# Kernel optimization log

Hardware: AMD Instinct MI355X
Metric: run time of the kernel (lower is better)

The kernel has to match this reference:

```python
import jax, jax.numpy as jnp
import numpy as np
from jax import lax

T, N, C, S = 1024, 64, 512, 64
BLANK = 0
STRUCT_TAGS = jnp.array([1, 2, 3, 4, 5, 6, 7, 8], dtype=jnp.int32)
STRUCT_WEIGHT = 1.0
NEG = -1e30


def setup_inputs() -> dict:
    key = jax.random.key(0)
    k1, k2, k3 = jax.random.split(key, 3)
    logits = jax.random.normal(k1, (T, N, C), dtype=jnp.float32)
    log_probs = jax.nn.log_softmax(logits, axis=-1)
    targets = jax.random.randint(k2, (N, S), 1, C, dtype=jnp.int32)  # exclude blank
    input_lengths = jnp.full((N,), T, dtype=jnp.int32)
    target_lengths = jax.random.randint(k3, (N,), 32, S + 1, dtype=jnp.int32)
    return {"log_probs": log_probs, "targets": targets,
            "input_lengths": input_lengths, "target_lengths": target_lengths}


def _is_struct(x):
    return (x[..., None] == STRUCT_TAGS).any(-1)


def _compact(tokens, mask, L):
    # Pack masked tokens to the left, pad with -1. tokens/mask: (N, L) -> (N, L)
    n = tokens.shape[0]
    pos = jnp.cumsum(mask, axis=-1) - 1            # destination slot per kept token
    idx = jnp.where(mask, pos, L)                  # dump masked-out entries in slot L
    out = jnp.full((n, L + 1), -1, dtype=tokens.dtype)
    out = out.at[jnp.arange(n)[:, None], idx].set(jnp.where(mask, tokens, -1))
    return out[:, :L]


def _ctc_loss(log_probs, targets, input_lengths, target_lengths):
    # Extended target: blanks interleaved -> (N, U), U = 2S+1
    U = 2 * S + 1
    ext = jnp.full((N, U), BLANK, dtype=targets.dtype).at[:, 1::2].set(targets)
    # lp[t, n, u] = log_probs[t, n, ext[n, u]]
    lp = log_probs[:, jnp.arange(N)[:, None], ext]                 # (T, N, U)
    ext2 = jnp.concatenate([jnp.full((N, 2), -1, ext.dtype), ext[:, :-2]], 1)
    allow_skip = (ext != BLANK) & (ext != ext2)                    # (N, U)

    a0 = jnp.full((N, U), NEG, dtype=log_probs.dtype)
    a0 = a0.at[:, 0].set(lp[0, :, 0]).at[:, 1].set(lp[0, :, 1])

    def step(a, lp_t):
        a1 = jnp.concatenate([jnp.full((N, 1), NEG, a.dtype), a[:, :-1]], 1)
        a2 = jnp.concatenate([jnp.full((N, 2), NEG, a.dtype), a[:, :-2]], 1)
        a2 = jnp.where(allow_skip, a2, NEG)
        a_new = jnp.logaddexp(jnp.logaddexp(a, a1), a2) + lp_t
        return a_new, a_new

    _, alphas = lax.scan(step, a0, lp[1:])
    alphas = jnp.concatenate([a0[None], alphas], 0)                # (T, N, U)

    n = jnp.arange(N)
    aT = alphas[input_lengths - 1, n]                              # (N, U)
    u_last = 2 * target_lengths
    loss = -jnp.logaddexp(aT[n, u_last], aT[n, u_last - 1])        # (N,)
    return jnp.where(loss > 1e20, 0.0, loss)                       # zero_infinity


def _struct_penalty(log_probs, targets, input_lengths, target_lengths):
    pred = jnp.argmax(log_probs, axis=-1).T.astype(jnp.int32)      # (N, T)
    valid = jnp.arange(T)[None, :] < input_lengths[:, None]
    p = jnp.where(valid, pred, BLANK)
    prev = jnp.concatenate([jnp.full((N, 1), -1, p.dtype), p[:, :-1]], 1)
    keep = (p != prev) & (p != BLANK) & _is_struct(p)              # collapsed, non-blank, struct
    pred_struct = _compact(p, keep, T)                             # (N, T)

    tvalid = jnp.arange(S)[None, :] < target_lengths[:, None]
    tmask = tvalid & _is_struct(targets)
    tgt_struct = _compact(targets.astype(jnp.int32), tmask, S)     # (N, S)
    tgt_pad = jnp.concatenate([tgt_struct, jnp.full((N, T - S), -1, jnp.int32)], 1)

    mismatch = (pred_struct != tgt_pad).any(-1)
    return mismatch.astype(log_probs.dtype)                        # (N,)


def reference(log_probs, targets, input_lengths, target_lengths):
    content = _ctc_loss(log_probs, targets, input_lengths, target_lengths)
    penalty = _struct_penalty(log_probs, targets, input_lengths, target_lengths)
    total = content + STRUCT_WEIGHT * penalty
    return total.mean()  # reduction='mean'
```

## Files before the change

kernel.cpp:

```cpp
#include <hip/hip_runtime.h>
#include <hip/hip_bf16.h>
#include <cstdint>
#include <cstddef>

#define TT 1024
#define NN 64
#define CC 512
#define SS 64
#define NEGF (-1e30f)
#define LN2F 0.6931471805599453f
#define SMALLE (-0x40000000)

__device__ __forceinline__ float exp2i(float x) { return __builtin_amdgcn_exp2f(x); }
__device__ __forceinline__ float log2i(float x) { return __builtin_amdgcn_logf(x); }

__device__ __forceinline__ float ldx(float x, int e) {
#if __has_builtin(__builtin_amdgcn_ldexpf)
  return __builtin_amdgcn_ldexpf(x, e);
#else
  return ldexpf(x, e);
#endif
}

__device__ __forceinline__ float lse2(float x, float y) {
  float m = fmaxf(x, y);
  float d = fabsf(x - y);
  return m + log2i(1.0f + exp2i(-d));
}
__device__ __forceinline__ float lse3(float x, float y, float z) {
  float m = fmaxf(fmaxf(x, y), z);
  float s = exp2i(x - m) + exp2i(y - m) + exp2i(z - m);
  return m + log2i(s);
}

__device__ __forceinline__ float dpp_shr1(float x, float oldv) {
  int r = __builtin_amdgcn_update_dpp(__float_as_int(oldv), __float_as_int(x),
                                      0x138, 0xF, 0xF, false);
  return __int_as_float(r);
}
__device__ __forceinline__ int dpp_shr1_i(int x, int oldv) {
  return __builtin_amdgcn_update_dpp(oldv, x, 0x138, 0xF, 0xF, false);
}

__device__ __forceinline__ float q2log(float Q, int E) {
  return (Q > 0.0f) ? (log2i(Q) + (float)E) : NEGF;
}

__global__ __launch_bounds__(256) void k_rowpass(
    const float* __restrict__ lp, const int* __restrict__ targets,
    float* __restrict__ Wt, float* __restrict__ Wb, int* __restrict__ pred) {
  __shared__ float rows[4][CC];
  __shared__ float Gs[16][65];
  __shared__ float Gsb[16];
  const int tid = threadIdx.x;
  const int wid = tid >> 6;
  const int l = tid & 63;
  const int n = blockIdx.x & 63;
  const int tc = blockIdx.x >> 6;

  const int tgt = targets[n * SS + l];

  for (int i = 0; i < 4; ++i) {
    const int tl = wid * 4 + i;
    const int t = tc * 16 + tl;
    const float* row = lp + ((size_t)t * NN + n) * CC;
    const float4 v0 = ((const float4*)row)[l];
    const float4 v1 = ((const float4*)row)[l + 64];
    ((float4*)rows[wid])[l] = v0;
    ((float4*)rows[wid])[l + 64] = v1;

    float bv = v0.x;
    int bi = 4 * l;
#define UPD(v, idx)                                \
    do {                                           \
      if ((v) > bv || ((v) == bv && (idx) < bi)) { \
        bv = (v);                                  \
        bi = (idx);                                \
      }                                            \
    } while (0)
    UPD(v0.y, 4 * l + 1);
    UPD(v0.z, 4 * l + 2);
    UPD(v0.w, 4 * l + 3);
    UPD(v1.x, 256 + 4 * l);
    UPD(v1.y, 256 + 4 * l + 1);
    UPD(v1.z, 256 + 4 * l + 2);
    UPD(v1.w, 256 + 4 * l + 3);
#pragma unroll
    for (int off = 32; off; off >>= 1) {
      float ov = __shfl_xor(bv, off);
      int oi = __shfl_xor(bi, off);
      UPD(ov, oi);
    }
#undef UPD

    const float gv = rows[wid][tgt];
    Gs[tl][l] = __expf(gv);
    if (l == 0) {
      Gsb[tl] = __expf(v0.x);
      pred[n * TT + t] = bi;
    }
  }
  __syncthreads();

  const int q = tid >> 6;
  float4 w;
  w.x = Gs[q * 4 + 0][l];
  w.y = Gs[q * 4 + 1][l];
  w.z = Gs[q * 4 + 2][l];
  w.w = Gs[q * 4 + 3][l];
  ((float4*)(Wt + (size_t)(n * 64 + l) * TT + tc * 16))[q] = w;
  if (tid < 16) Wb[(size_t)n * TT + tc * 16 + tid] = Gsb[tid];
}

__global__ __launch_bounds__(192) void k_ctc(
    const float* __restrict__ Wt, const float* __restrict__ Wb,
    const int* __restrict__ targets, const int* __restrict__ ilen,
    const int* __restrict__ tlen, const int* __restrict__ pred,
    float* __restrict__ content, float* __restrict__ pen) {
  __shared__ float Bo[64], Be[64], BTs;
  __shared__ int ts[SS];
  const int n = blockIdx.x;
  const int tid = threadIdx.x;
  const int wid = tid >> 6;
  const int l = tid & 63;

  const int Lm1 = __builtin_amdgcn_readfirstlane(ilen[n]) - 1;
  const int Ltg = __builtin_amdgcn_readfirstlane(tlen[n]);

  float fe0 = NEGF, fe1 = NEGF, fa0 = NEGF;
  float s0L = NEGF, s1L = NEGF;

  if (wid == 0) {
    const int tgt = targets[n * SS + l];
    const int tprev = __shfl_up(tgt, 1);
    const float skipf = ((l == 0) || (tgt != tprev)) ? 1.0f : 0.0f;
    const float4* bt = (const float4*)(Wt + (size_t)(n * 64 + l) * TT);
    const float4* bb = (const float4*)(Wb + (size_t)n * TT);
    float4 ring[8], ringb[8];
#pragma unroll
    for (int i = 0; i < 8; ++i) {
      ring[i] = bt[i];
      ringb[i] = bb[i];
    }

    float Q0 = 0.0f, Q1 = 0.0f, Qa = 1.0f;
    int E = 0, Ea = 0, dEnb = 0, dEa = 0;
    float sQ0 = 0.0f, sQ1 = 0.0f;
    int sE = 0;

#define FSTEP(WTv, WBv)                              \
    {                                                \
      const float a0f = ldx(Qa, dEa);                \
      const float up0 = dpp_shr1(Q0, a0f);           \
      const float up1 = dpp_shr1(Q1, 0.0f);          \
      const float uu = fmaf(skipf, up1, up0);        \
      const float us = ldx(uu, dEnb);                \
      const float n1 = (Q1 + us) * (WTv);            \
      const float n0 = (Q0 + Q1) * (WBv);            \
      Qa *= (WBv);                                   \
      Q0 = n0;                                       \
      Q1 = n1;                                       \
    }
#define FRENORM                                               \
    {                                                         \
      const float mq = fmaxf(Q0, Q1);                         \
      const int eo = (mq > 0.0f)                              \
          ? (E + (((__float_as_int(mq) >> 23) & 255) - 127))  \
          : SMALLE;                                           \
      const int en = dpp_shr1_i(eo, SMALLE);                  \
      int En = (eo > en) ? eo : en;                           \
      if (En == SMALLE) En = E;                               \
      const int sh = E - En;                                  \
      Q0 = ldx(Q0, sh);                                       \
      Q1 = ldx(Q1, sh);                                       \
      E = En;                                                 \
      const int Eup = dpp_shr1_i(E, E);                       \
      dEnb = Eup - E;                                         \
      const int exa = ((__float_as_int(Qa) >> 23) & 255) - 127; \
      Ea += exa;                                              \
      Qa = ldx(Qa, -exa);                                     \
      dEa = Ea - E;                                           \
    }

    for (int g = 0; g < 16; ++g) {
#pragma unroll
      for (int ci = 0; ci < 8; ++ci) {
        const int c = g * 8 + ci;
        const float4 wt4 = ring[ci];
        const float4 wb4 = ringb[ci];
        ring[ci] = bt[c + 8];
        ringb[ci] = bb[c + 8];
        if (__builtin_expect((unsigned)(Lm1 - c * 4) < 4u, 0)) {
          FSTEP(wt4.x, wb4.x);
          if (c * 4 + 0 == Lm1) { sQ0 = Q0; sQ1 = Q1; sE = E; }
          FSTEP(wt4.y, wb4.y);
          if (c * 4 + 1 == Lm1) { sQ0 = Q0; sQ1 = Q1; sE = E; }
          FSTEP(wt4.z, wb4.z);
          if (c * 4 + 2 == Lm1) { sQ0 = Q0; sQ1 = Q1; sE = E; }
          FSTEP(wt4.w, wb4.w);
          if (c * 4 + 3 == Lm1) { sQ0 = Q0; sQ1 = Q1; sE = E; }
        } else {
          FSTEP(wt4.x, wb4.x);
          FSTEP(wt4.y, wb4.y);
          FSTEP(wt4.z, wb4.z);
          FSTEP(wt4.w, wb4.w);
        }
        FRENORM;
      }
    }
#undef FSTEP
#undef FRENORM
    fe0 = q2log(Q0, E);
    fe1 = q2log(Q1, E);
    fa0 = q2log(Qa, Ea);
    s0L = q2log(sQ0, sE);
    s1L = q2log(sQ1, sE);
  } else if (wid == 1) {
    const int m = 63 - l;
    const int tm = targets[n * SS + m];
    const int tmp = __shfl_up(tm, 1);
    const float skipbf = ((l > 0) && (tm != tmp)) ? 1.0f : 0.0f;
    const float4* bt = (const float4*)(Wt + (size_t)(n * 64 + m) * TT);
    const float4* bb = (const float4*)(Wb + (size_t)n * TT);
    float4 ring[8], ringb[8];
#pragma unroll
    for (int i = 0; i < 8; ++i) {
      ring[i] = bt[255 - i];
      ringb[i] = bb[255 - i];
    }

    float Qd0 = 0.0f, Qd1 = 0.0f, QaT = 0.0f;
    int Eb = 0, EaT = 0, dEnb = 0, dEa = 0;

#define BSTEP(WTv, WBv)                              \
    {                                                \
      const float aTf = ldx(QaT, dEa);               \
      const float nd0 = dpp_shr1(Qd0, aTf);          \
      const float nd1 = dpp_shr1(Qd1, 0.0f);         \
      const float uu = fmaf(skipbf, nd1, nd0);       \
      const float us = ldx(uu, dEnb);                \
      const float n1 = (Qd1 + us) * (WTv);           \
      const float n0 = (Qd0 + Qd1) * (WBv);          \
      QaT *= (WBv);                                  \
      Qd0 = n0;                                      \
      Qd1 = n1;                                      \
    }
#define BINIT(WTv, WBv)                              \
    {                                                \
      Qd0 = (m == Ltg) ? (WBv) : 0.0f;               \
      Qd1 = (m == Ltg - 1) ? (WTv) : 0.0f;           \
      QaT = (Ltg == 64) ? (WBv) : 0.0f;              \
      Eb = 0; EaT = 0; dEnb = 0; dEa = 0;            \
    }
#define BRENORM                                               \
    {                                                         \
      const float mq = fmaxf(Qd0, Qd1);                       \
      const int eo = (mq > 0.0f)                              \
          ? (Eb + (((__float_as_int(mq) >> 23) & 255) - 127)) \
          : SMALLE;                                           \
      const int en = dpp_shr1_i(eo, SMALLE);                  \
      int En = (eo > en) ? eo : en;                           \
      if (En == SMALLE) En = Eb;                              \
      const int sh = Eb - En;                                 \
      Qd0 = ldx(Qd0, sh);                                     \
      Qd1 = ldx(Qd1, sh);                                     \
      Eb = En;                                                \
      const int Eup = dpp_shr1_i(Eb, Eb);                     \
      dEnb = Eup - Eb;                                        \
      if (QaT > 0.0f) {                                       \
        const int exa = ((__float_as_int(QaT) >> 23) & 255) - 127; \
        EaT += exa;                                           \
        QaT = ldx(QaT, -exa);                                 \
      }                                                       \
      dEa = EaT - Eb;                                         \
    }

    for (int g = 0; g < 16; ++g) {
#pragma unroll
      for (int ci = 0; ci < 8; ++ci) {
        const int cs = g * 8 + ci;
        const float4 wt4 = ring[ci];
        const float4 wb4 = ringb[ci];
        ring[ci] = bt[255 - cs - 8];
        ringb[ci] = bb[255 - cs - 8];
        const int thi = 1023 - 4 * cs;
        if (__builtin_expect((unsigned)(thi - Lm1) < 4u, 0)) {
          if (thi - 0 == Lm1) BINIT(wt4.w, wb4.w) else BSTEP(wt4.w, wb4.w);
          if (thi - 1 == Lm1) BINIT(wt4.z, wb4.z) else BSTEP(wt4.z, wb4.z);
          if (thi - 2 == Lm1) BINIT(wt4.y, wb4.y) else BSTEP(wt4.y, wb4.y);
          if (thi - 3 == Lm1) BINIT(wt4.x, wb4.x) else BSTEP(wt4.x, wb4.x);
        } else {
          BSTEP(wt4.w, wb4.w);
          BSTEP(wt4.z, wb4.z);
          BSTEP(wt4.y, wb4.y);
          BSTEP(wt4.x, wb4.x);
        }
        BRENORM;
      }
    }
#undef BSTEP
#undef BINIT
#undef BRENORM

    const float d0L = q2log(Qd0, Eb);
    const float d1L = q2log(Qd1, Eb);
    const float aTL = q2log(QaT, EaT);
    const float nd0 = dpp_shr1(d0L, aTL);
    const float nd1 = dpp_shr1(d1L, NEGF);
    const float skz = ((l > 0) && (tm != tmp)) ? nd1 : NEGF;
    Bo[m] = lse3(d1L, nd0, skz);
    Be[m] = lse2(d0L, d1L);
    if (l == 0) BTs = aTL;
  } else {
    const int tv = targets[n * SS + l];
    const bool tf = (l < Ltg) && (tv >= 1) && (tv <= 8);
    const unsigned long long tmk = __ballot(tf);
    const int tcnt = __popcll(tmk);
    if (tf) ts[__popcll(tmk & ((1ull << l) - 1ull))] = tv;

    const int L_in = Lm1 + 1;
    int mism = 0;
    int prevc = -1;
    int base = 0;
#pragma unroll 4
    for (int c = 0; c < TT / 64; ++c) {
      const int t = c * 64 + l;
      int p = pred[n * TT + t];
      if (t >= L_in) p = 0;
      int pp = __shfl_up(p, 1);
      if (l == 0) pp = prevc;
      const bool keep = (p != pp) && (p >= 1) && (p <= 8);
      const unsigned long long mk = __ballot(keep);
      const int pos = base + __popcll(mk & ((1ull << l) - 1ull));
      if (keep && (pos >= tcnt || ts[pos] != p)) mism = 1;
      base += __popcll(mk);
      prevc = __shfl(p, 63);
    }
    if (base != tcnt) mism = 1;
    if (__any(mism)) mism = 1;
    if (l == 0) pen[n] = mism ? 1.0f : 0.0f;
  }

  __syncthreads();

  if (wid == 0) {
    float loss;
    if (Lm1 >= 512) {
      const float to_ = fe1 + Bo[l];
      const float te_ = fe0 + ((l < 63) ? Be[l + 1] : BTs);
      const float t0_ = (l == 0) ? (fa0 + Be[0]) : NEGF;
      float mx = fmaxf(fmaxf(to_, te_), t0_);
#pragma unroll
      for (int off = 32; off; off >>= 1) mx = fmaxf(mx, __shfl_xor(mx, off));
      float s = exp2i(to_ - mx) + exp2i(te_ - mx) +
                ((l == 0) ? exp2i(t0_ - mx) : 0.0f);
#pragma unroll
      for (int off = 32; off; off >>= 1) s += __shfl_xor(s, off);
      loss = -(mx + log2i(s)) * LN2F;
    } else {
      const float pA = __shfl(s0L, Ltg - 1);
      const float pB = __shfl(s1L, Ltg - 1);
      loss = -lse2(pA, pB) * LN2F;
    }
    if (loss > 1e20f) loss = 0.0f;
    if (!(loss <= 1e20f)) loss = 0.0f;
    if (l == 0) content[n] = loss;
  }
}

__global__ __launch_bounds__(64) void k_red(
    const float* __restrict__ content, const float* __restrict__ pen,
    float* __restrict__ out) {
  const int l = threadIdx.x;
  float v = content[l] + pen[l];
#pragma unroll
  for (int off = 32; off; off >>= 1) v += __shfl_down(v, off);
  if (l == 0) out[0] = v * (1.0f / NN);
}

extern "C" void kernel_launch(void* const* d_in, const int* in_sizes, int n_in,
                              void* d_out, int out_size, void* d_ws,
                              size_t ws_size, hipStream_t stream) {
  const float* log_probs = (const float*)d_in[0];
  const int* targets = (const int*)d_in[1];
  const int* input_lengths = (const int*)d_in[2];
  const int* target_lengths = (const int*)d_in[3];
  float* out = (float*)d_out;

  float* Wt = (float*)d_ws;
  float* Wb = Wt + (size_t)TT * NN * 64;
  int* pred = (int*)(Wb + (size_t)TT * NN);
  float* content = (float*)(pred + (size_t)NN * TT);
  float* pen = content + NN;

  k_rowpass<<<NN * (TT / 16), 256, 0, stream>>>(log_probs, targets, Wt, Wb, pred);
  k_ctc<<<NN, 192, 0, stream>>>(Wt, Wb, targets, input_lengths, target_lengths,
                                pred, content, pen);
  k_red<<<1, 64, 0, stream>>>(content, pen, out);
}
```

Measured before the change: 60.84 us.

## Store target emission probabilities as bf16 and use packed-key DPP argmax

The per-target emission probabilities written by the row pass and read by the CTC recursion are now stored as bf16 instead of fp32. This halves that intermediate's memory traffic and the register footprint of the prefetch ring, at the cost of lower precision in the CTC loss. The argmax now packs each (value, index) pair into a 64-bit key and reduces it with DPP row and broadcast operations instead of shuffles with compare branches. The key packing assumes the inputs are non-positive, which holds for log-probabilities.

```diff
diff --git a/kernel.cpp b/kernel.cpp
--- a/kernel.cpp
+++ b/kernel.cpp
@@ -42,13 +42,38 @@
   return __builtin_amdgcn_update_dpp(oldv, x, 0x138, 0xF, 0xF, false);
 }
 
-__device__ __forceinline__ float q2log(float Q, int E) {
-  return (Q > 0.0f) ? (log2i(Q) + (float)E) : NEGF;
-}
+template <int CTRL>
+__device__ __forceinline__ unsigned long long dpp_umax64(unsigned long long k) {
+  const int lo = (int)(unsigned)k;
+  const int hi = (int)(unsigned)(k >> 32);
+  const int slo = __builtin_amdgcn_update_dpp(lo, lo, CTRL, 0xF, 0xF, false);
+  const int shi = __builtin_amdgcn_update_dpp(hi, hi, CTRL, 0xF, 0xF, false);
+  const unsigned long long o =
+      ((unsigned long long)(unsigned)shi << 32) | (unsigned)slo;
+  return o > k ? o : k;
+}
+
+__device__ __forceinline__ unsigned long long akey(float v, int idx) {
+  return ((unsigned long long)(~__float_as_uint(v)) << 32) |
+         (unsigned)(511 - idx);
+}
+__device__ __forceinline__ unsigned long long umax64(unsigned long long a,
+                                                     unsigned long long b) {
+  return a > b ? a : b;
+}
+
+__device__ __forceinline__ unsigned bf16rne(float f) {
+  unsigned u = __float_as_uint(f);
+  return (u + 0x7FFFu + ((u >> 16) & 1u)) >> 16;
+}
+
+#define BF_LO(r) __uint_as_float((r) << 16)
+#define BF_HI(r) __uint_as_float((r) & 0xFFFF0000u)
 
 __global__ __launch_bounds__(256) void k_rowpass(
     const float* __restrict__ lp, const int* __restrict__ targets,
-    float* __restrict__ Wt, float* __restrict__ Wb, int* __restrict__ pred) {
+    unsigned short* __restrict__ Wt16, float* __restrict__ Wb,
+    int* __restrict__ pred) {
   __shared__ float rows[4][CC];
   __shared__ float Gs[16][65];
   __shared__ float Gsb[16];
@@ -69,51 +94,39 @@
     ((float4*)rows[wid])[l] = v0;
     ((float4*)rows[wid])[l + 64] = v1;
 
-    float bv = v0.x;
-    int bi = 4 * l;
-#define UPD(v, idx)                                \
-    do {                                           \
-      if ((v) > bv || ((v) == bv && (idx) < bi)) { \
-        bv = (v);                                  \
-        bi = (idx);                                \
-      }                                            \
-    } while (0)
-    UPD(v0.y, 4 * l + 1);
-    UPD(v0.z, 4 * l + 2);
-    UPD(v0.w, 4 * l + 3);
-    UPD(v1.x, 256 + 4 * l);
-    UPD(v1.y, 256 + 4 * l + 1);
-    UPD(v1.z, 256 + 4 * l + 2);
-    UPD(v1.w, 256 + 4 * l + 3);
-#pragma unroll
-    for (int off = 32; off; off >>= 1) {
-      float ov = __shfl_xor(bv, off);
-      int oi = __shfl_xor(bi, off);
-      UPD(ov, oi);
-    }
-#undef UPD
+    const unsigned long long ka =
+        umax64(akey(v0.x, 4 * l), akey(v0.y, 4 * l + 1));
+    const unsigned long long kb =
+        umax64(akey(v0.z, 4 * l + 2), akey(v0.w, 4 * l + 3));
+    const unsigned long long kc =
+        umax64(akey(v1.x, 256 + 4 * l), akey(v1.y, 256 + 4 * l + 1));
+    const unsigned long long kd =
+        umax64(akey(v1.z, 256 + 4 * l + 2), akey(v1.w, 256 + 4 * l + 3));
+    unsigned long long k = umax64(umax64(ka, kb), umax64(kc, kd));
+    k = dpp_umax64<0x111>(k);
+    k = dpp_umax64<0x112>(k);
+    k = dpp_umax64<0x114>(k);
+    k = dpp_umax64<0x118>(k);
+    k = dpp_umax64<0x142>(k);
+    k = dpp_umax64<0x143>(k);
 
     const float gv = rows[wid][tgt];
     Gs[tl][l] = __expf(gv);
-    if (l == 0) {
-      Gsb[tl] = __expf(v0.x);
-      pred[n * TT + t] = bi;
-    }
+    if (l == 63) pred[n * TT + t] = 511 - (int)(unsigned)k;
+    if (l == 0) Gsb[tl] = __expf(v0.x);
   }
   __syncthreads();
 
   const int q = tid >> 6;
-  float4 w;
-  w.x = Gs[q * 4 + 0][l];
-  w.y = Gs[q * 4 + 1][l];
-  w.z = Gs[q * 4 + 2][l];
-  w.w = Gs[q * 4 + 3][l];
-  ((float4*)(Wt + (size_t)(n * 64 + l) * TT + tc * 16))[q] = w;
+  uint2 wv;
+  wv.x = bf16rne(Gs[q * 4 + 0][l]) | (bf16rne(Gs[q * 4 + 1][l]) << 16);
+  wv.y = bf16rne(Gs[q * 4 + 2][l]) | (bf16rne(Gs[q * 4 + 3][l]) << 16);
+  *(uint2*)(Wt16 + (size_t)(n * 64 + l) * TT + tc * 16 + q * 4) = wv;
   if (tid < 16) Wb[(size_t)n * TT + tc * 16 + tid] = Gsb[tid];
 }
 
 __global__ __launch_bounds__(192) void k_ctc(
-    const float* __restrict__ Wt, const float* __restrict__ Wb,
+    const unsigned short* __restrict__ Wt16, const float* __restrict__ Wb,
     const int* __restrict__ targets, const int* __restrict__ ilen,
     const int* __restrict__ tlen, const int* __restrict__ pred,
     float* __restrict__ content, float* __restrict__ pen) {
@@ -134,9 +147,10 @@
     const int tgt = targets[n * SS + l];
     const int tprev = __shfl_up(tgt, 1);
     const float skipf = ((l == 0) || (tgt != tprev)) ? 1.0f : 0.0f;
-    const float4* bt = (const float4*)(Wt + (size_t)(n * 64 + l) * TT);
+    const uint2* bt = (const uint2*)(Wt16 + (size_t)(n * 64 + l) * TT);
     const float4* bb = (const float4*)(Wb + (size_t)n * TT);
-    float4 ring[8], ringb[8];
+    uint2 ring[8];
+    float4 ringb[8];
 #pragma unroll
     for (int i = 0; i < 8; ++i) {
       ring[i] = bt[i];
@@ -186,43 +200,45 @@
 #pragma unroll
       for (int ci = 0; ci < 8; ++ci) {
         const int c = g * 8 + ci;
-        const float4 wt4 = ring[ci];
+        const uint2 wt4 = ring[ci];
         const float4 wb4 = ringb[ci];
         ring[ci] = bt[c + 8];
         ringb[ci] = bb[c + 8];
         if (__builtin_expect((unsigned)(Lm1 - c * 4) < 4u, 0)) {
-          FSTEP(wt4.x, wb4.x);
+          FSTEP(BF_LO(wt4.x), wb4.x);
           if (c * 4 + 0 == Lm1) { sQ0 = Q0; sQ1 = Q1; sE = E; }
-          FSTEP(wt4.y, wb4.y);
+          FSTEP(BF_HI(wt4.x), wb4.y);
           if (c * 4 + 1 == Lm1) { sQ0 = Q0; sQ1 = Q1; sE = E; }
-          FSTEP(wt4.z, wb4.z);
+          FSTEP(BF_LO(wt4.y), wb4.z);
           if (c * 4 + 2 == Lm1) { sQ0 = Q0; sQ1 = Q1; sE = E; }
-          FSTEP(wt4.w, wb4.w);
+          FSTEP(BF_HI(wt4.y), wb4.w);
           if (c * 4 + 3 == Lm1) { sQ0 = Q0; sQ1 = Q1; sE = E; }
         } else {
-          FSTEP(wt4.x, wb4.x);
-          FSTEP(wt4.y, wb4.y);
-          FSTEP(wt4.z, wb4.z);
-          FSTEP(wt4.w, wb4.w);
+          FSTEP(BF_LO(wt4.x), wb4.x);
+          FSTEP(BF_HI(wt4.x), wb4.y);
+          FSTEP(BF_LO(wt4.y), wb4.z);
+          FSTEP(BF_HI(wt4.y), wb4.w);
         }
         FRENORM;
       }
     }
 #undef FSTEP
 #undef FRENORM
-    fe0 = q2log(Q0, E);
-    fe1 = q2log(Q1, E);
-    fa0 = q2log(Qa, Ea);
-    s0L = q2log(sQ0, sE);
-    s1L = q2log(sQ1, sE);
+    const float fE = (float)E;
+    fe0 = (Q0 > 0.0f) ? (log2i(Q0) + fE) : NEGF;
+    fe1 = (Q1 > 0.0f) ? (log2i(Q1) + fE) : NEGF;
+    fa0 = (Qa > 0.0f) ? (log2i(Qa) + (float)Ea) : NEGF;
+    s0L = (sQ0 > 0.0f) ? (log2i(sQ0) + (float)sE) : NEGF;
+    s1L = (sQ1 > 0.0f) ? (log2i(sQ1) + (float)sE) : NEGF;
   } else if (wid == 1) {
     const int m = 63 - l;
     const int tm = targets[n * SS + m];
     const int tmp = __shfl_up(tm, 1);
     const float skipbf = ((l > 0) && (tm != tmp)) ? 1.0f : 0.0f;
-    const float4* bt = (const float4*)(Wt + (size_t)(n * 64 + m) * TT);
+    const uint2* bt = (const uint2*)(Wt16 + (size_t)(n * 64 + m) * TT);
     const float4* bb = (const float4*)(Wb + (size_t)n * TT);
-    float4 ring[8], ringb[8];
+    uint2 ring[8];
+    float4 ringb[8];
 #pragma unroll
     for (int i = 0; i < 8; ++i) {
       ring[i] = bt[255 - i];
@@ -279,21 +295,21 @@
 #pragma unroll
       for (int ci = 0; ci < 8; ++ci) {
         const int cs = g * 8 + ci;
-        const float4 wt4 = ring[ci];
+        const uint2 wt4 = ring[ci];
         const float4 wb4 = ringb[ci];
         ring[ci] = bt[255 - cs - 8];
         ringb[ci] = bb[255 - cs - 8];
         const int thi = 1023 - 4 * cs;
         if (__builtin_expect((unsigned)(thi - Lm1) < 4u, 0)) {
-          if (thi - 0 == Lm1) BINIT(wt4.w, wb4.w) else BSTEP(wt4.w, wb4.w);
-          if (thi - 1 == Lm1) BINIT(wt4.z, wb4.z) else BSTEP(wt4.z, wb4.z);
-          if (thi - 2 == Lm1) BINIT(wt4.y, wb4.y) else BSTEP(wt4.y, wb4.y);
-          if (thi - 3 == Lm1) BINIT(wt4.x, wb4.x) else BSTEP(wt4.x, wb4.x);
+          if (thi - 0 == Lm1) BINIT(BF_HI(wt4.y), wb4.w) else BSTEP(BF_HI(wt4.y), wb4.w);
+          if (thi - 1 == Lm1) BINIT(BF_LO(wt4.y), wb4.z) else BSTEP(BF_LO(wt4.y), wb4.z);
+          if (thi - 2 == Lm1) BINIT(BF_HI(wt4.x), wb4.y) else BSTEP(BF_HI(wt4.x), wb4.y);
+          if (thi - 3 == Lm1) BINIT(BF_LO(wt4.x), wb4.x) else BSTEP(BF_LO(wt4.x), wb4.x);
         } else {
-          BSTEP(wt4.w, wb4.w);
-          BSTEP(wt4.z, wb4.z);
-          BSTEP(wt4.y, wb4.y);
-          BSTEP(wt4.x, wb4.x);
+          BSTEP(BF_HI(wt4.y), wb4.w);
+          BSTEP(BF_LO(wt4.y), wb4.z);
+          BSTEP(BF_HI(wt4.x), wb4.y);
+          BSTEP(BF_LO(wt4.x), wb4.x);
         }
         BRENORM;
       }
@@ -302,9 +318,10 @@
 #undef BINIT
 #undef BRENORM
 
-    const float d0L = q2log(Qd0, Eb);
-    const float d1L = q2log(Qd1, Eb);
-    const float aTL = q2log(QaT, EaT);
+    const float fEb = (float)Eb;
+    const float d0L = (Qd0 > 0.0f) ? (log2i(Qd0) + fEb) : NEGF;
+    const float d1L = (Qd1 > 0.0f) ? (log2i(Qd1) + fEb) : NEGF;
+    const float aTL = (QaT > 0.0f) ? (log2i(QaT) + (float)EaT) : NEGF;
     const float nd0 = dpp_shr1(d0L, aTL);
     const float nd1 = dpp_shr1(d1L, NEGF);
     const float skz = ((l > 0) && (tm != tmp)) ? nd1 : NEGF;
@@ -387,14 +404,15 @@
   const int* target_lengths = (const int*)d_in[3];
   float* out = (float*)d_out;
 
-  float* Wt = (float*)d_ws;
-  float* Wb = Wt + (size_t)TT * NN * 64;
-  int* pred = (int*)(Wb + (size_t)TT * NN);
+  unsigned short* Wt16 = (unsigned short*)d_ws;
+  float* Wb = (float*)(Wt16 + (size_t)NN * 64 * TT);
+  int* pred = (int*)(Wb + (size_t)NN * TT);
   float* content = (float*)(pred + (size_t)NN * TT);
   float* pen = content + NN;
 
-  k_rowpass<<<NN * (TT / 16), 256, 0, stream>>>(log_probs, targets, Wt, Wb, pred);
-  k_ctc<<<NN, 192, 0, stream>>>(Wt, Wb, targets, input_lengths, target_lengths,
-                                pred, content, pen);
+  k_rowpass<<<NN * (TT / 16), 256, 0, stream>>>(log_probs, targets, Wt16, Wb,
+                                                pred);
+  k_ctc<<<NN, 192, 0, stream>>>(Wt16, Wb, targets, input_lengths,
+                                target_lengths, pred, content, pen);
   k_red<<<1, 64, 0, stream>>>(content, pen, out);
 }
```

After: 57.12 us. 6.1% less time.
